# Performance work log

Measured on AMD Instinct MI355X. Metric: run time of the kernel, lower is better.

## Reference

```python
import jax, jax.numpy as jnp
import numpy as np

N, M, D = 2048, 16, 256


def setup_inputs() -> dict:
    key = jax.random.key(0)
    k1, = jax.random.split(key, 1)
    embeddings = jax.random.normal(k1, (N, M, D), dtype=jnp.float32)
    w = jnp.asarray(10.0, dtype=jnp.float32)
    b = jnp.asarray(-5.0, dtype=jnp.float32)
    return {"embeddings": embeddings, "w": w, "b": b}


def reference(embeddings, w, b):
    # embeddings: [N, M, D]
    centroids = embeddings.mean(axis=1)          # [N, D]
    sum_ = embeddings.sum(axis=1)                # [N, D]
    e = embeddings.reshape(N * M, D)             # [NM, D]
    cosine_sim = e @ centroids.T                 # [NM, N]
    # excluded-self centroid for each (speaker j, utterance i):
    # cj = (sum_[j] - e_ji) / (M - 1); replace cosine_sim[ji, j] with dot(cj, e_ji)
    excl = (sum_[:, None, :] - embeddings) / (M - 1)           # [N, M, D]
    diag_vals = jnp.sum(excl * embeddings, axis=-1).reshape(N * M)  # [NM]
    labels = jnp.repeat(jnp.arange(N), M)                      # [NM]
    cosine_sim = cosine_sim.at[jnp.arange(N * M), labels].set(diag_vals)
    logits = w * cosine_sim + b                                # [NM, N]
    logp = jax.nn.log_softmax(logits, axis=-1)
    loss = -jnp.mean(logp[jnp.arange(N * M), labels])
    return loss
```

## Files before the change

kernel.cpp:

```cpp
#include <hip/hip_runtime.h>
#include <hip/hip_bf16.h>
#if !__has_builtin(__builtin_amdgcn_cvt_pk_fp8_f32)
#include <hip/hip_fp8.h>
#endif

#define NS 2048
#define MU 16
#define DD 256
#define NMROWS (NS*MU)
#define STRIPS 8
#define SC 256
#define NSTEP 4
#define BMROWS 128
#define THR 8.0f

typedef float  f32x4  __attribute__((ext_vector_type(4)));
typedef float  f32x16 __attribute__((ext_vector_type(16)));
typedef int    i32x4  __attribute__((ext_vector_type(4)));
typedef int    i32x8  __attribute__((ext_vector_type(8)));

#define LOG2E 1.44269504088896340736f
#define LN2   0.69314718055994530942f

#if __has_builtin(__builtin_amdgcn_exp2f)
#define EXP2F(x) __builtin_amdgcn_exp2f(x)
#else
#define EXP2F(x) exp2f(x)
#endif
#if __has_builtin(__builtin_amdgcn_logf)
#define LOG2F(x) __builtin_amdgcn_logf(x)
#else
#define LOG2F(x) __log2f(x)
#endif

__device__ __forceinline__ int pk4(float a, float b, float c, float d){
#if __has_builtin(__builtin_amdgcn_cvt_pk_fp8_f32)
  int v = __builtin_amdgcn_cvt_pk_fp8_f32(a, b, 0, false);
  v = __builtin_amdgcn_cvt_pk_fp8_f32(c, d, v, true);
  return v;
#else
  unsigned r = (unsigned)__hip_fp8_e4m3(a).__x
             | ((unsigned)__hip_fp8_e4m3(b).__x << 8)
             | ((unsigned)__hip_fp8_e4m3(c).__x << 16)
             | ((unsigned)__hip_fp8_e4m3(d).__x << 24);
  return (int)r;
#endif
}


__launch_bounds__(256)
__global__ void prep_kernel(const float* __restrict__ emb,
                            const float* __restrict__ wp,
                            i32x4* __restrict__ centk16,
                            unsigned char* __restrict__ embk8,
                            float* __restrict__ diag2){
  __shared__ float E[16*260];
  __shared__ float sm[256];
  const int t = threadIdx.x;
  const int n = blockIdx.x;
  const float* src = emb + (size_t)n*MU*DD;

  #pragma unroll
  for (int i=0;i<4;i++){
    int g = i*1024 + t*4;
    f32x4 v = *(const f32x4*)(src + g);
    int m = g >> 8, d = g & 255;
    *(f32x4*)&E[m*260 + d] = v;
  }
  __syncthreads();

  {
    float s = 0.f;
    #pragma unroll
    for (int m=0;m<16;m++) s += E[m*260 + t];
    sm[t] = s;
  }
  __syncthreads();

  const float w2 = wp[0] * LOG2E;

  if (t < 16){
    const float c16 = w2 * (1.0f/16.0f);
    const int st = t;
    const float* p = &sm[st*16];
    i32x4 o;
    #pragma unroll
    for (int q=0;q<4;q++)
      o[q] = pk4(p[q*4]*c16, p[q*4+1]*c16, p[q*4+2]*c16, p[q*4+3]*c16);
    centk16[(size_t)st*NS + n] = o;
  }

  if (embk8){
    int st = t >> 4, r = t & 15;
    const float* p = &E[r*260 + st*16];
    i32x4 o;
    #pragma unroll
    for (int q=0;q<4;q++){
      f32x4 v = *(const f32x4*)(p + q*4);
      o[q] = pk4(v[0], v[1], v[2], v[3]);
    }
    *(i32x4*)(embk8 + ((size_t)st*NMROWS + n*16 + r)*16) = o;
  }

  {
    int m = t >> 4, j = t & 15;
    float acc = 0.f;
    #pragma unroll
    for (int i=0;i<16;i++){
      int d = j + 16*i;
      float e = E[m*260 + d];
      acc += e * (sm[d] - e);
    }
    acc += __shfl_xor(acc, 1, 16);
    acc += __shfl_xor(acc, 2, 16);
    acc += __shfl_xor(acc, 4, 16);
    acc += __shfl_xor(acc, 8, 16);
    if (j==0) diag2[n*16 + m] = acc * (w2 * (1.0f/15.0f));
  }
}

__device__ __forceinline__ void stage_b(const i32x4* __restrict__ centk16,
                                        i32x4* lds, int col0,
                                        int wave, int lane){
  #pragma unroll
  for (int i=0;i<4;i++){
    const int st = i*4 + wave;
    const i32x4* g = centk16 + (size_t)st*NS + col0 + lane;
    __builtin_amdgcn_global_load_lds(
        (const __attribute__((address_space(1))) void*)g,
        (__attribute__((address_space(3))) void*)(lds + (size_t)st*64),
        16, 0, 0);
  }
}

#define MFMAS(a,b,c) __builtin_amdgcn_mfma_scale_f32_32x32x64_f8f6f4( \
    a, b, c, 0, 0, 0, 0x7f7f7f7fu, 0, 0x7f7f7f7fu)

template<bool FROMF32>
__launch_bounds__(256,4)
__global__ void ge2e_main(const float* __restrict__ embf,
                          const unsigned char* __restrict__ embk8,
                          const i32x4* __restrict__ centk16,
                          const float* __restrict__ diag2,
                          float2* __restrict__ msbuf){
  __shared__ i32x4 Bbuf[2][1024];

  const int tid  = threadIdx.x;
  const int lane = tid & 63;
  const int wave = tid >> 6;
  const int l31  = lane & 31, hi = lane >> 5;
  const int strip  = blockIdx.x & 7;
  const int rowBlk = blockIdx.x >> 3;
  const int c0 = strip * SC;
  const int rowA = rowBlk*BMROWS + wave*32 + l31;

  stage_b(centk16, &Bbuf[0][0], c0, wave, lane);

  i32x8 af[4];
  if constexpr (FROMF32){
    const float* rp = embf + (size_t)rowA*DD;
    #pragma unroll
    for (int c=0;c<4;c++){
      i32x8 o;
      #pragma unroll
      for (int h=0;h<2;h++){
        const float* q = rp + (4*c + 2*hi + h)*16;
        #pragma unroll
        for (int j=0;j<4;j++)
          o[h*4+j] = pk4(q[j*4], q[j*4+1], q[j*4+2], q[j*4+3]);
      }
      af[c] = o;
    }
  } else {
    #pragma unroll
    for (int c=0;c<4;c++){
      i32x4 x = *(const i32x4*)(embk8 + ((size_t)(4*c+2*hi  )*NMROWS + rowA)*16);
      i32x4 y = *(const i32x4*)(embk8 + ((size_t)(4*c+2*hi+1)*NMROWS + rowA)*16);
      i32x8 o; o[0]=x[0];o[1]=x[1];o[2]=x[2];o[3]=x[3];
               o[4]=y[0];o[5]=y[1];o[6]=y[2];o[7]=y[3];
      af[c] = o;
    }
  }

  const float dv  = diag2[rowA];
  const int   lab = rowA >> 4;
  const int   labc0 = rowBlk*8;
  const bool  hasdiag = (labc0 >= c0) && (labc0 < c0 + SC);
  const int   dstep = (labc0 - c0) >> 6;
  const int   dgrp  = ((labc0 - c0) >> 5) & 1;

  float mneg = 0.f, s = 0.f;

  __syncthreads();

  for (int step=0; step<NSTEP; ++step){
    const int cb_ = step & 1;
    if (step+1 < NSTEP)
      stage_b(centk16, &Bbuf[cb_^1][0], c0 + (step+1)*64, wave, lane);

    const i32x4* cur = &Bbuf[cb_][0];

    f32x16 ci;
    #pragma unroll
    for (int i=0;i<16;i++) ci[i] = mneg;

    f32x16 accA = ci, accB = ci;
    #pragma unroll
    for (int c=0;c<4;c++){
      i32x4 a0 = cur[(4*c+2*hi  )*64      + l31];
      i32x4 a1 = cur[(4*c+2*hi+1)*64      + l31];
      i32x4 b0 = cur[(4*c+2*hi  )*64 + 32 + l31];
      i32x4 b1 = cur[(4*c+2*hi+1)*64 + 32 + l31];
      i32x8 bA; bA[0]=a0[0];bA[1]=a0[1];bA[2]=a0[2];bA[3]=a0[3];
                bA[4]=a1[0];bA[5]=a1[1];bA[6]=a1[2];bA[7]=a1[3];
      i32x8 bB; bB[0]=b0[0];bB[1]=b0[1];bB[2]=b0[2];bB[3]=b0[3];
                bB[4]=b1[0];bB[5]=b1[1];bB[6]=b1[2];bB[7]=b1[3];
      accA = MFMAS(bA, af[c], accA);
      accB = MFMAS(bB, af[c], accB);
    }

    if (hasdiag && step == dstep){
      int colbase = c0 + step*64 + dgrp*32 + 4*hi;
      if (dgrp == 0){
        #pragma unroll
        for (int r=0;r<16;r++){
          int col = colbase + (r&3) + 8*(r>>2);
          if (col == lab) accA[r] = dv + mneg;
        }
      } else {
        #pragma unroll
        for (int r=0;r<16;r++){
          int col = colbase + (r&3) + 8*(r>>2);
          if (col == lab) accB[r] = dv + mneg;
        }
      }
    }

    float xa0 = fmaxf(fmaxf(fmaxf(accA[0],accA[1]),fmaxf(accA[2],accA[3])),
                      fmaxf(fmaxf(accA[4],accA[5]),fmaxf(accA[6],accA[7])));
    float xa1 = fmaxf(fmaxf(fmaxf(accA[8],accA[9]),fmaxf(accA[10],accA[11])),
                      fmaxf(fmaxf(accA[12],accA[13]),fmaxf(accA[14],accA[15])));
    float xb0 = fmaxf(fmaxf(fmaxf(accB[0],accB[1]),fmaxf(accB[2],accB[3])),
                      fmaxf(fmaxf(accB[4],accB[5]),fmaxf(accB[6],accB[7])));
    float xb1 = fmaxf(fmaxf(fmaxf(accB[8],accB[9]),fmaxf(accB[10],accB[11])),
                      fmaxf(fmaxf(accB[12],accB[13]),fmaxf(accB[14],accB[15])));
    float tm = fmaxf(fmaxf(xa0,xa1), fmaxf(xb0,xb1));

    if (__any(tm > THR)){
      float d = fmaxf(tm, 0.f);
      s *= EXP2F(-d);
      mneg -= d;
      float a0=0.f, b0=0.f;
      #pragma unroll
      for (int r=0;r<16;r++){ a0 += EXP2F(accA[r]-d); b0 += EXP2F(accB[r]-d); }
      s += a0 + b0;
    } else {
      float a0 = EXP2F(accA[0])+EXP2F(accA[1])+EXP2F(accA[2])+EXP2F(accA[3]);
      float a1 = EXP2F(accA[4])+EXP2F(accA[5])+EXP2F(accA[6])+EXP2F(accA[7]);
      float a2 = EXP2F(accA[8])+EXP2F(accA[9])+EXP2F(accA[10])+EXP2F(accA[11]);
      float a3 = EXP2F(accA[12])+EXP2F(accA[13])+EXP2F(accA[14])+EXP2F(accA[15]);
      float b0 = EXP2F(accB[0])+EXP2F(accB[1])+EXP2F(accB[2])+EXP2F(accB[3]);
      float b1 = EXP2F(accB[4])+EXP2F(accB[5])+EXP2F(accB[6])+EXP2F(accB[7]);
      float b2 = EXP2F(accB[8])+EXP2F(accB[9])+EXP2F(accB[10])+EXP2F(accB[11]);
      float b3 = EXP2F(accB[12])+EXP2F(accB[13])+EXP2F(accB[14])+EXP2F(accB[15]);
      s += ((a0+a1)+(a2+a3)) + ((b0+b1)+(b2+b3));
    }

    asm volatile("s_waitcnt vmcnt(0)" ::: "memory");
    __builtin_amdgcn_s_barrier();
  }

  float m  = -mneg;
  float mo = __shfl_xor(m,32,64), so = __shfl_xor(s,32,64);
  float mm = fmaxf(m,mo);
  float ss = s*EXP2F(m-mm) + so*EXP2F(mo-mm);

  if (hi==0) msbuf[(size_t)strip*NMROWS + rowA] = make_float2(mm, ss);
}

__launch_bounds__(512)
__global__ void merge_kernel(const float2* __restrict__ msbuf,
                             const float* __restrict__ diag2,
                             float* __restrict__ partials){
  __shared__ float sh[8];
  const int row = blockIdx.x*512 + threadIdx.x;
  float2 p[STRIPS];
  #pragma unroll
  for (int k=0;k<STRIPS;k++) p[k] = msbuf[(size_t)k*NMROWS + row];
  float mm = p[0].x;
  #pragma unroll
  for (int k=1;k<STRIPS;k++) mm = fmaxf(mm, p[k].x);
  float ss = 0.f;
  #pragma unroll
  for (int k=0;k<STRIPS;k++) ss += p[k].y * EXP2F(p[k].x - mm);
  float term = LN2*(mm + LOG2F(ss) - diag2[row]);
  #pragma unroll
  for (int off=32; off; off>>=1) term += __shfl_xor(term, off, 64);
  if ((threadIdx.x & 63)==0) sh[threadIdx.x>>6] = term;
  __syncthreads();
  if (threadIdx.x==0){
    float v = 0.f;
    #pragma unroll
    for (int i=0;i<8;i++) v += sh[i];
    partials[blockIdx.x] = v;
  }
}

__global__ void final_kernel(const float* __restrict__ partials,
                             float* __restrict__ out){
  int tid = threadIdx.x;
  float v = partials[tid];
  #pragma unroll
  for (int off=32; off; off>>=1) v += __shfl_xor(v, off, 64);
  if (tid==0) out[0] = v * (1.0f/NMROWS);
}

extern "C" void kernel_launch(void* const* d_in, const int* in_sizes, int n_in,
                              void* d_out, int out_size, void* d_ws, size_t ws_size,
                              hipStream_t stream){
  const float* emb = (const float*)d_in[0];
  const float* wp  = (const float*)d_in[1];
  float* out = (float*)d_out;
  char* ws = (char*)d_ws;

  const size_t centk_b = (size_t)NS*DD;
  const size_t embk_b  = (size_t)NMROWS*DD;
  const size_t diag_b  = (size_t)NMROWS*4;
  const size_t ms_b    = (size_t)STRIPS*NMROWS*8;
  const bool useEmbk = ws_size >= centk_b + embk_b + diag_b + ms_b + 1024;

  i32x4* centk16 = (i32x4*)ws;
  size_t off = centk_b;
  unsigned char* embk8 = useEmbk ? (unsigned char*)(ws + off) : nullptr;
  if (useEmbk) off += embk_b;
  float*  diag2 = (float*)(ws + off);  off += diag_b;
  float2* msbuf = (float2*)(ws + off); off += ms_b;
  float*  parts = (float*)(ws + off);

  prep_kernel<<<NS, 256, 0, stream>>>(emb, wp, centk16, embk8, diag2);
  if (useEmbk)
    ge2e_main<false><<<(NMROWS/BMROWS)*STRIPS, 256, 0, stream>>>(emb, embk8, centk16, diag2, msbuf);
  else
    ge2e_main<true><<<(NMROWS/BMROWS)*STRIPS, 256, 0, stream>>>(emb, embk8, centk16, diag2, msbuf);
  merge_kernel<<<NMROWS/512, 512, 0, stream>>>(msbuf, diag2, parts);
  final_kernel<<<1, 64, 0, stream>>>(parts, out);
}
```

Baseline: 41.61 us.

## Double rows per wave to reuse staged centroid tiles across two row sets

Result: no change. 41.45 us, median of 2 (-0.4%).

```diff
diff --git a/kernel.cpp b/kernel.cpp
--- a/kernel.cpp
+++ b/kernel.cpp
@@ -11,7 +11,7 @@
 #define STRIPS 8
 #define SC 256
 #define NSTEP 4
-#define BMROWS 128
+#define BMROWS 256
 #define THR 8.0f
 
 typedef float  f32x4  __attribute__((ext_vector_type(4)));
@@ -47,6 +47,15 @@
 #endif
 }
 
+__device__ __forceinline__ float max16(const f32x16& v){
+  float t0 = fmaxf(fmaxf(v[0], v[1]), v[2]);
+  float t1 = fmaxf(fmaxf(v[3], v[4]), v[5]);
+  float t2 = fmaxf(fmaxf(v[6], v[7]), v[8]);
+  float t3 = fmaxf(fmaxf(v[9], v[10]), v[11]);
+  float t4 = fmaxf(fmaxf(v[12], v[13]), v[14]);
+  return fmaxf(fmaxf(fmaxf(t0, t1), t2), fmaxf(fmaxf(t3, t4), v[15]));
+}
+
 
 __launch_bounds__(256)
 __global__ void prep_kernel(const float* __restrict__ emb,
@@ -137,7 +146,7 @@
     a, b, c, 0, 0, 0, 0x7f7f7f7fu, 0, 0x7f7f7f7fu)
 
 template<bool FROMF32>
-__launch_bounds__(256,4)
+__launch_bounds__(256,3)
 __global__ void ge2e_main(const float* __restrict__ embf,
                           const unsigned char* __restrict__ embk8,
                           const i32x4* __restrict__ centk16,
@@ -153,43 +162,54 @@
   const int rowBlk = blockIdx.x >> 3;
   const int c0 = strip * SC;
   const int rowA = rowBlk*BMROWS + wave*32 + l31;
+  const int rowB = rowA + 128;
 
   stage_b(centk16, &Bbuf[0][0], c0, wave, lane);
 
-  i32x8 af[4];
+  i32x8 af0[4], af1[4];
   if constexpr (FROMF32){
-    const float* rp = embf + (size_t)rowA*DD;
     #pragma unroll
     for (int c=0;c<4;c++){
-      i32x8 o;
+      i32x8 o0, o1;
       #pragma unroll
       for (int h=0;h<2;h++){
-        const float* q = rp + (4*c + 2*hi + h)*16;
+        const float* q0 = embf + (size_t)rowA*DD + (4*c + 2*hi + h)*16;
+        const float* q1 = embf + (size_t)rowB*DD + (4*c + 2*hi + h)*16;
         #pragma unroll
-        for (int j=0;j<4;j++)
-          o[h*4+j] = pk4(q[j*4], q[j*4+1], q[j*4+2], q[j*4+3]);
+        for (int j=0;j<4;j++){
+          o0[h*4+j] = pk4(q0[j*4], q0[j*4+1], q0[j*4+2], q0[j*4+3]);
+          o1[h*4+j] = pk4(q1[j*4], q1[j*4+1], q1[j*4+2], q1[j*4+3]);
+        }
       }
-      af[c] = o;
+      af0[c]=o0; af1[c]=o1;
     }
   } else {
     #pragma unroll
     for (int c=0;c<4;c++){
-      i32x4 x = *(const i32x4*)(embk8 + ((size_t)(4*c+2*hi  )*NMROWS + rowA)*16);
-      i32x4 y = *(const i32x4*)(embk8 + ((size_t)(4*c+2*hi+1)*NMROWS + rowA)*16);
-      i32x8 o; o[0]=x[0];o[1]=x[1];o[2]=x[2];o[3]=x[3];
-               o[4]=y[0];o[5]=y[1];o[6]=y[2];o[7]=y[3];
-      af[c] = o;
-    }
-  }
-
-  const float dv  = diag2[rowA];
-  const int   lab = rowA >> 4;
-  const int   labc0 = rowBlk*8;
+      i32x4 x0 = *(const i32x4*)(embk8 + ((size_t)(4*c+2*hi  )*NMROWS + rowA)*16);
+      i32x4 y0 = *(const i32x4*)(embk8 + ((size_t)(4*c+2*hi+1)*NMROWS + rowA)*16);
+      i32x4 x1 = *(const i32x4*)(embk8 + ((size_t)(4*c+2*hi  )*NMROWS + rowB)*16);
+      i32x4 y1 = *(const i32x4*)(embk8 + ((size_t)(4*c+2*hi+1)*NMROWS + rowB)*16);
+      i32x8 o0; o0[0]=x0[0];o0[1]=x0[1];o0[2]=x0[2];o0[3]=x0[3];
+                o0[4]=y0[0];o0[5]=y0[1];o0[6]=y0[2];o0[7]=y0[3];
+      i32x8 o1; o1[0]=x1[0];o1[1]=x1[1];o1[2]=x1[2];o1[3]=x1[3];
+                o1[4]=y1[0];o1[5]=y1[1];o1[6]=y1[2];o1[7]=y1[3];
+      af0[c]=o0; af1[c]=o1;
+    }
+  }
+
+  const float dv0 = diag2[rowA], dv1 = diag2[rowB];
+  const int   lab0 = rowA >> 4, lab1 = rowB >> 4;
+  const int   labc0 = rowBlk*16;
   const bool  hasdiag = (labc0 >= c0) && (labc0 < c0 + SC);
   const int   dstep = (labc0 - c0) >> 6;
-  const int   dgrp  = ((labc0 - c0) >> 5) & 1;
-
-  float mneg = 0.f, s = 0.f;
+  const int   dcg   = ((labc0 - c0) >> 5) & 1;
+
+  f32x16 zz;
+  #pragma unroll
+  for (int i=0;i<16;i++) zz[i] = 0.f;
+
+  float m0 = -3.0e38f, s0 = 0.f, m1 = -3.0e38f, s1 = 0.f;
 
   __syncthreads();
 
@@ -200,82 +220,69 @@
 
     const i32x4* cur = &Bbuf[cb_][0];
 
-    f32x16 ci;
-    #pragma unroll
-    for (int i=0;i<16;i++) ci[i] = mneg;
-
-    f32x16 accA = ci, accB = ci;
-    #pragma unroll
-    for (int c=0;c<4;c++){
-      i32x4 a0 = cur[(4*c+2*hi  )*64      + l31];
-      i32x4 a1 = cur[(4*c+2*hi+1)*64      + l31];
-      i32x4 b0 = cur[(4*c+2*hi  )*64 + 32 + l31];
-      i32x4 b1 = cur[(4*c+2*hi+1)*64 + 32 + l31];
-      i32x8 bA; bA[0]=a0[0];bA[1]=a0[1];bA[2]=a0[2];bA[3]=a0[3];
-                bA[4]=a1[0];bA[5]=a1[1];bA[6]=a1[2];bA[7]=a1[3];
-      i32x8 bB; bB[0]=b0[0];bB[1]=b0[1];bB[2]=b0[2];bB[3]=b0[3];
-                bB[4]=b1[0];bB[5]=b1[1];bB[6]=b1[2];bB[7]=b1[3];
-      accA = MFMAS(bA, af[c], accA);
-      accB = MFMAS(bB, af[c], accB);
-    }
-
-    if (hasdiag && step == dstep){
-      int colbase = c0 + step*64 + dgrp*32 + 4*hi;
-      if (dgrp == 0){
+    #pragma unroll
+    for (int cg=0; cg<2; ++cg){
+      f32x16 accA, accB;
+      {
+        i32x4 x = cur[(2*hi  )*64 + cg*32 + l31];
+        i32x4 y = cur[(2*hi+1)*64 + cg*32 + l31];
+        i32x8 bb; bb[0]=x[0];bb[1]=x[1];bb[2]=x[2];bb[3]=x[3];
+                  bb[4]=y[0];bb[5]=y[1];bb[6]=y[2];bb[7]=y[3];
+        accA = MFMAS(bb, af0[0], zz);
+        accB = MFMAS(bb, af1[0], zz);
+      }
+      #pragma unroll
+      for (int c=1;c<4;c++){
+        i32x4 x = cur[(4*c+2*hi  )*64 + cg*32 + l31];
+        i32x4 y = cur[(4*c+2*hi+1)*64 + cg*32 + l31];
+        i32x8 bb; bb[0]=x[0];bb[1]=x[1];bb[2]=x[2];bb[3]=x[3];
+                  bb[4]=y[0];bb[5]=y[1];bb[6]=y[2];bb[7]=y[3];
+        accA = MFMAS(bb, af0[c], accA);
+        accB = MFMAS(bb, af1[c], accB);
+      }
+
+      if (hasdiag && step == dstep && cg == dcg){
+        int colbase = c0 + step*64 + cg*32 + 4*hi;
         #pragma unroll
         for (int r=0;r<16;r++){
           int col = colbase + (r&3) + 8*(r>>2);
-          if (col == lab) accA[r] = dv + mneg;
-        }
-      } else {
-        #pragma unroll
-        for (int r=0;r<16;r++){
-          int col = colbase + (r&3) + 8*(r>>2);
-          if (col == lab) accB[r] = dv + mneg;
+          if (col == lab0) accA[r] = dv0;
+          if (col == lab1) accB[r] = dv1;
         }
       }
-    }
-
-    float xa0 = fmaxf(fmaxf(fmaxf(accA[0],accA[1]),fmaxf(accA[2],accA[3])),
-                      fmaxf(fmaxf(accA[4],accA[5]),fmaxf(accA[6],accA[7])));
-    float xa1 = fmaxf(fmaxf(fmaxf(accA[8],accA[9]),fmaxf(accA[10],accA[11])),
-                      fmaxf(fmaxf(accA[12],accA[13]),fmaxf(accA[14],accA[15])));
-    float xb0 = fmaxf(fmaxf(fmaxf(accB[0],accB[1]),fmaxf(accB[2],accB[3])),
-                      fmaxf(fmaxf(accB[4],accB[5]),fmaxf(accB[6],accB[7])));
-    float xb1 = fmaxf(fmaxf(fmaxf(accB[8],accB[9]),fmaxf(accB[10],accB[11])),
-                      fmaxf(fmaxf(accB[12],accB[13]),fmaxf(accB[14],accB[15])));
-    float tm = fmaxf(fmaxf(xa0,xa1), fmaxf(xb0,xb1));
-
-    if (__any(tm > THR)){
-      float d = fmaxf(tm, 0.f);
-      s *= EXP2F(-d);
-      mneg -= d;
-      float a0=0.f, b0=0.f;
-      #pragma unroll
-      for (int r=0;r<16;r++){ a0 += EXP2F(accA[r]-d); b0 += EXP2F(accB[r]-d); }
-      s += a0 + b0;
-    } else {
-      float a0 = EXP2F(accA[0])+EXP2F(accA[1])+EXP2F(accA[2])+EXP2F(accA[3]);
-      float a1 = EXP2F(accA[4])+EXP2F(accA[5])+EXP2F(accA[6])+EXP2F(accA[7]);
-      float a2 = EXP2F(accA[8])+EXP2F(accA[9])+EXP2F(accA[10])+EXP2F(accA[11]);
-      float a3 = EXP2F(accA[12])+EXP2F(accA[13])+EXP2F(accA[14])+EXP2F(accA[15]);
-      float b0 = EXP2F(accB[0])+EXP2F(accB[1])+EXP2F(accB[2])+EXP2F(accB[3]);
-      float b1 = EXP2F(accB[4])+EXP2F(accB[5])+EXP2F(accB[6])+EXP2F(accB[7]);
-      float b2 = EXP2F(accB[8])+EXP2F(accB[9])+EXP2F(accB[10])+EXP2F(accB[11]);
-      float b3 = EXP2F(accB[12])+EXP2F(accB[13])+EXP2F(accB[14])+EXP2F(accB[15]);
-      s += ((a0+a1)+(a2+a3)) + ((b0+b1)+(b2+b3));
+
+      float tmA = max16(accA);
+      float tmB = max16(accB);
+      if (__any(tmA > m0 + THR)){ float mn = fmaxf(m0,tmA); s0 *= EXP2F(m0-mn); m0 = mn; }
+      if (__any(tmB > m1 + THR)){ float mn = fmaxf(m1,tmB); s1 *= EXP2F(m1-mn); m1 = mn; }
+      float a0 = EXP2F(accA[0]-m0)+EXP2F(accA[1]-m0)+EXP2F(accA[2]-m0)+EXP2F(accA[3]-m0);
+      float a1 = EXP2F(accA[4]-m0)+EXP2F(accA[5]-m0)+EXP2F(accA[6]-m0)+EXP2F(accA[7]-m0);
+      float a2 = EXP2F(accA[8]-m0)+EXP2F(accA[9]-m0)+EXP2F(accA[10]-m0)+EXP2F(accA[11]-m0);
+      float a3 = EXP2F(accA[12]-m0)+EXP2F(accA[13]-m0)+EXP2F(accA[14]-m0)+EXP2F(accA[15]-m0);
+      s0 += (a0+a1)+(a2+a3);
+      float b0 = EXP2F(accB[0]-m1)+EXP2F(accB[1]-m1)+EXP2F(accB[2]-m1)+EXP2F(accB[3]-m1);
+      float b1 = EXP2F(accB[4]-m1)+EXP2F(accB[5]-m1)+EXP2F(accB[6]-m1)+EXP2F(accB[7]-m1);
+      float b2 = EXP2F(accB[8]-m1)+EXP2F(accB[9]-m1)+EXP2F(accB[10]-m1)+EXP2F(accB[11]-m1);
+      float b3 = EXP2F(accB[12]-m1)+EXP2F(accB[13]-m1)+EXP2F(accB[14]-m1)+EXP2F(accB[15]-m1);
+      s1 += (b0+b1)+(b2+b3);
     }
 
     asm volatile("s_waitcnt vmcnt(0)" ::: "memory");
     __builtin_amdgcn_s_barrier();
   }
 
-  float m  = -mneg;
-  float mo = __shfl_xor(m,32,64), so = __shfl_xor(s,32,64);
-  float mm = fmaxf(m,mo);
-  float ss = s*EXP2F(m-mm) + so*EXP2F(mo-mm);
-
-  if (hi==0) msbuf[(size_t)strip*NMROWS + rowA] = make_float2(mm, ss);
+  {
+    float mo = __shfl_xor(m0,32,64), so = __shfl_xor(s0,32,64);
+    float mm = fmaxf(m0,mo);
+    float ss = s0*EXP2F(m0-mm) + so*EXP2F(mo-mm);
+    if (hi==0) msbuf[(size_t)strip*NMROWS + rowA] = make_float2(mm, ss);
+  }
+  {
+    float mo = __shfl_xor(m1,32,64), so = __shfl_xor(s1,32,64);
+    float mm = fmaxf(m1,mo);
+    float ss = s1*EXP2F(m1-mm) + so*EXP2F(mo-mm);
+    if (hi==0) msbuf[(size_t)strip*NMROWS + rowB] = make_float2(mm, ss);
+  }
 }
 
 __launch_bounds__(512)
```

## Split MFMA chains into independent accumulators and simplify online-softmax rescaling

Applied to the files above, without the earlier changes.

After: 59.73 us. +43.5%, slower.

```diff
diff --git a/kernel.cpp b/kernel.cpp
--- a/kernel.cpp
+++ b/kernel.cpp
@@ -47,6 +47,15 @@
 #endif
 }
 
+__device__ __forceinline__ float max16(const f32x16& v){
+  float t0 = fmaxf(fmaxf(v[0], v[1]), v[2]);
+  float t1 = fmaxf(fmaxf(v[3], v[4]), v[5]);
+  float t2 = fmaxf(fmaxf(v[6], v[7]), v[8]);
+  float t3 = fmaxf(fmaxf(v[9], v[10]), v[11]);
+  float t4 = fmaxf(fmaxf(v[12], v[13]), v[14]);
+  return fmaxf(fmaxf(fmaxf(t0, t1), t2), fmaxf(fmaxf(t3, t4), v[15]));
+}
+
 
 __launch_bounds__(256)
 __global__ void prep_kernel(const float* __restrict__ emb,
@@ -136,8 +145,13 @@
 #define MFMAS(a,b,c) __builtin_amdgcn_mfma_scale_f32_32x32x64_f8f6f4( \
     a, b, c, 0, 0, 0, 0x7f7f7f7fu, 0, 0x7f7f7f7fu)
 
+#define LOADB(dst, c, cg) do { \
+    ((i32x4*)&(dst))[0] = cur[(4*(c)+2*hi  )*64 + (cg)*32 + l31]; \
+    ((i32x4*)&(dst))[1] = cur[(4*(c)+2*hi+1)*64 + (cg)*32 + l31]; \
+  } while(0)
+
 template<bool FROMF32>
-__launch_bounds__(256,4)
+__launch_bounds__(256,3)
 __global__ void ge2e_main(const float* __restrict__ embf,
                           const unsigned char* __restrict__ embk8,
                           const i32x4* __restrict__ centk16,
@@ -174,10 +188,9 @@
   } else {
     #pragma unroll
     for (int c=0;c<4;c++){
-      i32x4 x = *(const i32x4*)(embk8 + ((size_t)(4*c+2*hi  )*NMROWS + rowA)*16);
-      i32x4 y = *(const i32x4*)(embk8 + ((size_t)(4*c+2*hi+1)*NMROWS + rowA)*16);
-      i32x8 o; o[0]=x[0];o[1]=x[1];o[2]=x[2];o[3]=x[3];
-               o[4]=y[0];o[5]=y[1];o[6]=y[2];o[7]=y[3];
+      i32x8 o;
+      ((i32x4*)&o)[0] = *(const i32x4*)(embk8 + ((size_t)(4*c+2*hi  )*NMROWS + rowA)*16);
+      ((i32x4*)&o)[1] = *(const i32x4*)(embk8 + ((size_t)(4*c+2*hi+1)*NMROWS + rowA)*16);
       af[c] = o;
     }
   }
@@ -187,12 +200,13 @@
   const int   labc0 = rowBlk*8;
   const bool  hasdiag = (labc0 >= c0) && (labc0 < c0 + SC);
   const int   dstep = (labc0 - c0) >> 6;
-  const int   dgrp  = ((labc0 - c0) >> 5) & 1;
-
-  float mneg = 0.f, s = 0.f;
+  const int   dcg   = ((labc0 - c0) >> 5) & 1;
+
+  float m = -3.0e38f, s = 0.f;
 
   __syncthreads();
 
+  #pragma unroll
   for (int step=0; step<NSTEP; ++step){
     const int cb_ = step & 1;
     if (step+1 < NSTEP)
@@ -200,77 +214,65 @@
 
     const i32x4* cur = &Bbuf[cb_][0];
 
-    f32x16 ci;
-    #pragma unroll
-    for (int i=0;i<16;i++) ci[i] = mneg;
-
-    f32x16 accA = ci, accB = ci;
-    #pragma unroll
-    for (int c=0;c<4;c++){
-      i32x4 a0 = cur[(4*c+2*hi  )*64      + l31];
-      i32x4 a1 = cur[(4*c+2*hi+1)*64      + l31];
-      i32x4 b0 = cur[(4*c+2*hi  )*64 + 32 + l31];
-      i32x4 b1 = cur[(4*c+2*hi+1)*64 + 32 + l31];
-      i32x8 bA; bA[0]=a0[0];bA[1]=a0[1];bA[2]=a0[2];bA[3]=a0[3];
-                bA[4]=a1[0];bA[5]=a1[1];bA[6]=a1[2];bA[7]=a1[3];
-      i32x8 bB; bB[0]=b0[0];bB[1]=b0[1];bB[2]=b0[2];bB[3]=b0[3];
-                bB[4]=b1[0];bB[5]=b1[1];bB[6]=b1[2];bB[7]=b1[3];
-      accA = MFMAS(bA, af[c], accA);
-      accB = MFMAS(bB, af[c], accB);
-    }
+    f32x16 zz;
+    #pragma unroll
+    for (int i=0;i<16;i++) zz[i] = 0.f;
+
+    f32x16 a0, a1, b0, b1;
+    i32x8 v00, v01, v20, v21, v10, v11, v30, v31;
+    LOADB(v00, 0, 0);  LOADB(v01, 0, 1);
+    LOADB(v20, 2, 0);  LOADB(v21, 2, 1);
+    a0 = MFMAS(v00, af[0], zz);
+    b0 = MFMAS(v01, af[0], zz);
+    a1 = MFMAS(v20, af[2], zz);
+    b1 = MFMAS(v21, af[2], zz);
+    LOADB(v10, 1, 0);  LOADB(v11, 1, 1);
+    LOADB(v30, 3, 0);  LOADB(v31, 3, 1);
+    a0 = MFMAS(v10, af[1], a0);
+    b0 = MFMAS(v11, af[1], b0);
+    a1 = MFMAS(v30, af[3], a1);
+    b1 = MFMAS(v31, af[3], b1);
+
+    f32x16 accA = a0 + a1;
+    f32x16 accB = b0 + b1;
 
     if (hasdiag && step == dstep){
-      int colbase = c0 + step*64 + dgrp*32 + 4*hi;
-      if (dgrp == 0){
+      int colbase = c0 + step*64 + dcg*32 + 4*hi;
+      if (dcg == 0){
         #pragma unroll
         for (int r=0;r<16;r++){
           int col = colbase + (r&3) + 8*(r>>2);
-          if (col == lab) accA[r] = dv + mneg;
+          if (col == lab) accA[r] = dv;
         }
       } else {
         #pragma unroll
         for (int r=0;r<16;r++){
           int col = colbase + (r&3) + 8*(r>>2);
-          if (col == lab) accB[r] = dv + mneg;
+          if (col == lab) accB[r] = dv;
         }
       }
     }
 
-    float xa0 = fmaxf(fmaxf(fmaxf(accA[0],accA[1]),fmaxf(accA[2],accA[3])),
-                      fmaxf(fmaxf(accA[4],accA[5]),fmaxf(accA[6],accA[7])));
-    float xa1 = fmaxf(fmaxf(fmaxf(accA[8],accA[9]),fmaxf(accA[10],accA[11])),
-                      fmaxf(fmaxf(accA[12],accA[13]),fmaxf(accA[14],accA[15])));
-    float xb0 = fmaxf(fmaxf(fmaxf(accB[0],accB[1]),fmaxf(accB[2],accB[3])),
-                      fmaxf(fmaxf(accB[4],accB[5]),fmaxf(accB[6],accB[7])));
-    float xb1 = fmaxf(fmaxf(fmaxf(accB[8],accB[9]),fmaxf(accB[10],accB[11])),
-                      fmaxf(fmaxf(accB[12],accB[13]),fmaxf(accB[14],accB[15])));
-    float tm = fmaxf(fmaxf(xa0,xa1), fmaxf(xb0,xb1));
-
-    if (__any(tm > THR)){
-      float d = fmaxf(tm, 0.f);
-      s *= EXP2F(-d);
-      mneg -= d;
-      float a0=0.f, b0=0.f;
-      #pragma unroll
-      for (int r=0;r<16;r++){ a0 += EXP2F(accA[r]-d); b0 += EXP2F(accB[r]-d); }
-      s += a0 + b0;
-    } else {
-      float a0 = EXP2F(accA[0])+EXP2F(accA[1])+EXP2F(accA[2])+EXP2F(accA[3]);
-      float a1 = EXP2F(accA[4])+EXP2F(accA[5])+EXP2F(accA[6])+EXP2F(accA[7]);
-      float a2 = EXP2F(accA[8])+EXP2F(accA[9])+EXP2F(accA[10])+EXP2F(accA[11]);
-      float a3 = EXP2F(accA[12])+EXP2F(accA[13])+EXP2F(accA[14])+EXP2F(accA[15]);
-      float b0 = EXP2F(accB[0])+EXP2F(accB[1])+EXP2F(accB[2])+EXP2F(accB[3]);
-      float b1 = EXP2F(accB[4])+EXP2F(accB[5])+EXP2F(accB[6])+EXP2F(accB[7]);
-      float b2 = EXP2F(accB[8])+EXP2F(accB[9])+EXP2F(accB[10])+EXP2F(accB[11]);
-      float b3 = EXP2F(accB[12])+EXP2F(accB[13])+EXP2F(accB[14])+EXP2F(accB[15]);
-      s += ((a0+a1)+(a2+a3)) + ((b0+b1)+(b2+b3));
-    }
+    float tm = fmaxf(max16(accA), max16(accB));
+    if (__any(tm > m + THR)){
+      float mn = fmaxf(m, tm);
+      s *= EXP2F(m - mn);
+      m = mn;
+    }
+    float e0 = EXP2F(accA[0]-m)+EXP2F(accA[1]-m)+EXP2F(accA[2]-m)+EXP2F(accA[3]-m);
+    float e1 = EXP2F(accA[4]-m)+EXP2F(accA[5]-m)+EXP2F(accA[6]-m)+EXP2F(accA[7]-m);
+    float e2 = EXP2F(accA[8]-m)+EXP2F(accA[9]-m)+EXP2F(accA[10]-m)+EXP2F(accA[11]-m);
+    float e3 = EXP2F(accA[12]-m)+EXP2F(accA[13]-m)+EXP2F(accA[14]-m)+EXP2F(accA[15]-m);
+    float f0 = EXP2F(accB[0]-m)+EXP2F(accB[1]-m)+EXP2F(accB[2]-m)+EXP2F(accB[3]-m);
+    float f1 = EXP2F(accB[4]-m)+EXP2F(accB[5]-m)+EXP2F(accB[6]-m)+EXP2F(accB[7]-m);
+    float f2 = EXP2F(accB[8]-m)+EXP2F(accB[9]-m)+EXP2F(accB[10]-m)+EXP2F(accB[11]-m);
+    float f3 = EXP2F(accB[12]-m)+EXP2F(accB[13]-m)+EXP2F(accB[14]-m)+EXP2F(accB[15]-m);
+    s += ((e0+e1)+(e2+e3)) + ((f0+f1)+(f2+f3));
 
     asm volatile("s_waitcnt vmcnt(0)" ::: "memory");
     __builtin_amdgcn_s_barrier();
   }
 
-  float m  = -mneg;
   float mo = __shfl_xor(m,32,64), so = __shfl_xor(s,32,64);
   float mm = fmaxf(m,mo);
   float ss = s*EXP2F(m-mm) + so*EXP2F(mo-mm);
```
